# Kernel tuning notes

Hardware: AMD Instinct MI355X
Metric: run time of the kernel (lower is better)

Reference implementation:

```python
import jax, jax.numpy as jnp
import numpy as np

B, C, N, H = 4, 256, 4096, 4
DK = C // H


def _proj(x, w, b):
    # Conv1d with kernel size 1 == per-point linear: [B,C,N] x [O,C] -> [B,O,N]
    return jnp.einsum('oc,bcn->bon', w, x) + b[None, :, None]


def setup_inputs() -> dict:
    key = jax.random.key(0)
    ks = jax.random.split(key, 9)
    s = 1.0 / np.sqrt(C)
    return {
        'x': jax.random.normal(ks[0], (B, C, N), jnp.float32),
        'wq': jax.random.normal(ks[1], (C, C), jnp.float32) * s,
        'bq': jax.random.normal(ks[2], (C,), jnp.float32) * 0.01,
        'wk': jax.random.normal(ks[3], (C, C), jnp.float32) * s,
        'bk': jax.random.normal(ks[4], (C,), jnp.float32) * 0.01,
        'wv': jax.random.normal(ks[5], (C, C), jnp.float32) * s,
        'bv': jax.random.normal(ks[6], (C,), jnp.float32) * 0.01,
        'wp': jax.random.normal(ks[7], (C, C), jnp.float32) * s,
        'bp': jax.random.normal(ks[8], (C,), jnp.float32) * 0.01,
    }


def reference(x, wq, bq, wk, bk, wv, bv, wp, bp):
    b, c, n = x.shape
    q = _proj(x, wq, bq).reshape(b, H, DK, n)
    k = _proj(x, wk, bk).reshape(b, H, DK, n)
    v = _proj(x, wv, bv).reshape(b, H, DK, n)
    scale = 1.0 / jnp.sqrt(jnp.asarray(DK, x.dtype))
    # scores over point pairs: [B,H,N,N]
    scores = jnp.einsum('bhdn,bhdm->bhnm', q, k) * scale
    attn = jax.nn.softmax(scores, axis=-1)
    out = jnp.einsum('bhnm,bhdm->bhdn', attn, v)  # [B,H,DK,N]
    out = out.reshape(b, c, n)
    out = _proj(out, wp, bp)
    return out + x
```

## Files before the change

kernel.cpp:

```cpp
#include <hip/hip_runtime.h>


#define BDIM 4
#define CDIM 256
#define NDIM 4096
#define HDIM 4
#define DKDIM 64
#define NQ   (BDIM * HDIM * NDIM)
#define NSPLIT 2
#define KPERZ (NDIM / NSPLIT)
#define QSCALE 0.18033688011112042f
#define WSZ (CDIM * CDIM)

typedef __bf16 bf16x8 __attribute__((ext_vector_type(8)));
typedef float f32x4 __attribute__((ext_vector_type(4)));
typedef short s16x4 __attribute__((ext_vector_type(4)));
typedef unsigned short u16;
typedef unsigned int u32;

__device__ __forceinline__ u16 f2bf(float f) {
  union { __bf16 h; u16 s; } u; u.h = (__bf16)f; return u.s;
}
__device__ __forceinline__ float bf2f(u16 v) {
  union { u32 u; float f; } x; x.u = (u32)v << 16; return x.f;
}
__device__ __forceinline__ u32 pk2(float a, float b) {
  return (u32)f2bf(a) | ((u32)f2bf(b) << 16);
}
__device__ __forceinline__ void gload16(const u16* g, u16* l) {
  __builtin_amdgcn_global_load_lds(
      (const __attribute__((address_space(1))) void*)g,
      (__attribute__((address_space(3))) void*)l, 16, 0, 0);
}

__global__ __launch_bounds__(256) void wconv_kernel(
    const float* __restrict__ wq, const float* __restrict__ wk,
    const float* __restrict__ wv, const float* __restrict__ wp,
    u16* __restrict__ wb)
{
  const int a = blockIdx.y;
  const float* src = (a == 0) ? wq : (a == 1) ? wk : (a == 2) ? wv : wp;
  const float sc = (a == 0) ? QSCALE : 1.0f;
  const int i = (blockIdx.x * 256 + threadIdx.x) * 8;
  const float4 v0 = *(const float4*)(src + i);
  const float4 v1 = *(const float4*)(src + i + 4);
  union { u32 p[4]; uint4 q; } o;
  o.p[0] = pk2(v0.x * sc, v0.y * sc);
  o.p[1] = pk2(v0.z * sc, v0.w * sc);
  o.p[2] = pk2(v1.x * sc, v1.y * sc);
  o.p[3] = pk2(v1.z * sc, v1.w * sc);
  *(uint4*)(wb + (size_t)a * WSZ + i) = o.q;
}

__global__ __launch_bounds__(256) void xt_kernel(
    const float* __restrict__ x, u16* __restrict__ xT)
{
  const int b = blockIdx.z, c0 = blockIdx.y * 64, n0 = blockIdx.x * 64;
  __shared__ __align__(16) float T[64][68];
  const int t = threadIdx.x;
  {
    const int cr = t >> 4, nc = (t & 15) * 4;
    #pragma unroll
    for (int ci = 0; ci < 4; ++ci) {
      const float4 v = *(const float4*)&x[((size_t)(b * CDIM + c0 + cr + ci * 16)) * NDIM + n0 + nc];
      *(float4*)&T[cr + ci * 16][nc] = v;
    }
  }
  __syncthreads();
  {
    const int n = t >> 2, g = t & 3;
    union { u16 u[16]; uint4 v[2]; } pk;
    #pragma unroll
    for (int u_ = 0; u_ < 16; ++u_) pk.u[u_] = f2bf(T[g * 16 + u_][n]);
    uint4* dst = (uint4*)&xT[((size_t)(b * NDIM + n0 + n)) * CDIM + c0 + g * 16];
    dst[0] = pk.v[0]; dst[1] = pk.v[1];
  }
}

__global__ __launch_bounds__(256, 4) void qkv_kernel(
    const u16* __restrict__ xT, const u16* __restrict__ wb,
    const float* __restrict__ bq, const float* __restrict__ bk,
    const float* __restrict__ bv,
    u16* __restrict__ qT, u16* __restrict__ kT, u16* __restrict__ vB)
{
  const int b = blockIdx.z;
  const int p = blockIdx.y >> 1;
  const int o0 = (blockIdx.y & 1) * 128;
  const int n0 = blockIdx.x * 64;
  const float* bsel = (p == 0) ? bq : (p == 1) ? bk : bv;
  const float wscale = (p == 0) ? QSCALE : 1.0f;

  __shared__ __align__(16) u16 XTs[64][40];
  const int t = threadIdx.x, lane = t & 63, w = t >> 6;
  const int qd = lane >> 4, lm = lane & 15;
  const int sr = t >> 2, sg = (t & 3) * 8;

  const u16* xsrc = xT + ((size_t)(b * NDIM + n0 + sr)) * CDIM + sg;
  const u16* wrow0 = wb + (size_t)p * WSZ + (size_t)(o0 + 32 * w + lm) * CDIM + qd * 8;
  const u16* wrow1 = wrow0 + (size_t)16 * CDIM;

  f32x4 acc[4][2];
  #pragma unroll
  for (int nt = 0; nt < 4; ++nt)
    #pragma unroll
    for (int j = 0; j < 2; ++j) acc[nt][j] = (f32x4){0.f, 0.f, 0.f, 0.f};

  for (int cs = 0; cs < 8; ++cs) {
    const bf16x8 wf0 = *(const bf16x8*)(wrow0 + cs * 32);
    const bf16x8 wf1 = *(const bf16x8*)(wrow1 + cs * 32);
    __syncthreads();
    *(uint4*)&XTs[sr][sg] = *(const uint4*)(xsrc + cs * 32);
    __syncthreads();
    bf16x8 xf[4];
    #pragma unroll
    for (int nt = 0; nt < 4; ++nt) xf[nt] = *(const bf16x8*)&XTs[16 * nt + lm][qd * 8];
    #pragma unroll
    for (int nt = 0; nt < 4; ++nt) {
      if (p < 2) {
        acc[nt][0] = __builtin_amdgcn_mfma_f32_16x16x32_bf16(xf[nt], wf0, acc[nt][0], 0, 0, 0);
        acc[nt][1] = __builtin_amdgcn_mfma_f32_16x16x32_bf16(xf[nt], wf1, acc[nt][1], 0, 0, 0);
      } else {
        acc[nt][0] = __builtin_amdgcn_mfma_f32_16x16x32_bf16(wf0, xf[nt], acc[nt][0], 0, 0, 0);
        acc[nt][1] = __builtin_amdgcn_mfma_f32_16x16x32_bf16(wf1, xf[nt], acc[nt][1], 0, 0, 0);
      }
    }
  }

  if (p < 2) {
    u16* out = (p == 0) ? qT : kT;
    #pragma unroll
    for (int j = 0; j < 2; ++j) {
      const int og = o0 + 32 * w + 16 * j + lm;
      const float bv2 = bsel[og] * wscale;
      #pragma unroll
      for (int nt = 0; nt < 4; ++nt)
        #pragma unroll
        for (int r = 0; r < 4; ++r) {
          const int n = n0 + 16 * nt + 4 * qd + r;
          out[((size_t)(b * NDIM + n)) * CDIM + og] = f2bf(acc[nt][j][r] + bv2);
        }
    }
  } else {
    #pragma unroll
    for (int j = 0; j < 2; ++j) {
      const float4 b4 = *(const float4*)&bsel[o0 + 32 * w + 16 * j + 4 * qd];
      const float bvr[4] = {b4.x, b4.y, b4.z, b4.w};
      #pragma unroll
      for (int nt = 0; nt < 4; ++nt)
        #pragma unroll
        for (int r = 0; r < 4; ++r) {
          const int og = o0 + 32 * w + 16 * j + 4 * qd + r;
          const int n = n0 + 16 * nt + lm;
          vB[((size_t)(b * CDIM + og)) * NDIM + n] = f2bf(acc[nt][j][r] + bvr[r]);
        }
    }
  }
}

__global__ __launch_bounds__(256, 4) void attn_kernel(
    const u16* __restrict__ qT, const u16* __restrict__ kT,
    const u16* __restrict__ vB, u16* __restrict__ Opart,
    float* __restrict__ Lp)
{
  const int bh = blockIdx.y, b = bh >> 2, h = bh & 3;
  const int n0 = blockIdx.x * 128;
  const int z  = blockIdx.z;

  __shared__ __align__(16) u16 KVlds[2][2][64][64];

  const int t = threadIdx.x, lane = t & 63, w = t >> 6;
  const int qd = lane >> 4, lm = lane & 15, l7 = lm & 7;

  bf16x8 qf[2][2];
  {
    const u16* qbase = qT + ((size_t)(b * NDIM) + n0) * CDIM + h * 64;
    #pragma unroll
    for (int s = 0; s < 2; ++s)
      #pragma unroll
      for (int hh = 0; hh < 2; ++hh)
        qf[s][hh] = *(const bf16x8*)(qbase +
            (size_t)(16 * (2 * w + s) + lm) * CDIM + 32 * hh + qd * 8);
  }

  const s16x4 ones = (s16x4){(short)0x3F80, (short)0x3F80, (short)0x3F80, (short)0x3F80};
  f32x4 la[2];
  la[0] = (f32x4){0.f, 0.f, 0.f, 0.f};
  la[1] = (f32x4){0.f, 0.f, 0.f, 0.f};

  f32x4 oa[2][4];
  #pragma unroll
  for (int s = 0; s < 2; ++s)
    #pragma unroll
    for (int dt = 0; dt < 4; ++dt) oa[s][dt] = (f32x4){0.f, 0.f, 0.f, 0.f};

  const int srow = lane >> 3;
  const int swz  = 8 * ((lane & 7) ^ srow);
  const u16* kp0 = kT + ((size_t)(b * NDIM + z * KPERZ + 8 * w + srow)) * CDIM + h * 64 + swz;
  const u16* kp1 = kp0 + (size_t)32 * CDIM;
  const u16* vp0 = vB + ((size_t)(b * CDIM + h * 64 + 8 * w + srow)) * NDIM + z * KPERZ + swz;
  const u16* vp1 = vp0 + (size_t)32 * NDIM;

  {
    u16* kb = &KVlds[0][0][0][0];
    u16* vb2 = &KVlds[0][1][0][0];
    gload16(kp0, kb + w * 512);
    gload16(kp1, kb + (4 + w) * 512);
    gload16(vp0, vb2 + w * 512);
    gload16(vp1, vb2 + (4 + w) * 512);
  }

  #pragma unroll 1
  for (int it = 0; it < KPERZ / 64; ++it) {
    __syncthreads();
    if (it + 1 < KPERZ / 64) {
      const size_t ko = (size_t)(it + 1) * 64 * CDIM;
      const int    vo = (it + 1) * 64;
      u16* kb = &KVlds[(it + 1) & 1][0][0][0];
      u16* vb2 = &KVlds[(it + 1) & 1][1][0][0];
      gload16(kp0 + ko, kb + w * 512);
      gload16(kp1 + ko, kb + (4 + w) * 512);
      gload16(vp0 + vo, vb2 + w * 512);
      gload16(vp1 + vo, vb2 + (4 + w) * 512);
    }
    const u16 (*Kt)[64] = KVlds[it & 1][0];
    const u16 (*Vt)[64] = KVlds[it & 1][1];

    union { u16 u[4]; u32 d[2]; s16x4 v; } pk[2][4];

    #pragma unroll
    for (int nt = 0; nt < 4; ++nt) {
      const bf16x8 kf0 = *(const bf16x8*)&Kt[16 * nt + lm][8 * (qd ^ l7)];
      const bf16x8 kf1 = *(const bf16x8*)&Kt[16 * nt + lm][8 * ((4 + qd) ^ l7)];
      #pragma unroll
      for (int s = 0; s < 2; ++s) {
        f32x4 zz = (f32x4){0.f, 0.f, 0.f, 0.f};
        zz = __builtin_amdgcn_mfma_f32_16x16x32_bf16(kf0, qf[s][0], zz, 0, 0, 0);
        zz = __builtin_amdgcn_mfma_f32_16x16x32_bf16(kf1, qf[s][1], zz, 0, 0, 0);
        const float p0 = __builtin_amdgcn_exp2f(zz[0]);
        const float p1 = __builtin_amdgcn_exp2f(zz[1]);
        const float p2 = __builtin_amdgcn_exp2f(zz[2]);
        const float p3 = __builtin_amdgcn_exp2f(zz[3]);
        pk[s][nt].d[0] = pk2(p0, p1);
        pk[s][nt].d[1] = pk2(p2, p3);
      }
    }

    #pragma unroll
    for (int c = 0; c < 4; ++c) {
      s16x4 av[4];
      #pragma unroll
      for (int dt = 0; dt < 4; ++dt)
        av[dt] = *(const s16x4*)&Vt[16 * dt + lm][(16 * c + 4 * qd) ^ (8 * l7)];
      la[0] = __builtin_amdgcn_mfma_f32_16x16x16bf16_1k(ones, pk[0][c].v, la[0], 0, 0, 0);
      la[1] = __builtin_amdgcn_mfma_f32_16x16x16bf16_1k(ones, pk[1][c].v, la[1], 0, 0, 0);
      #pragma unroll
      for (int dt = 0; dt < 4; ++dt) {
        oa[0][dt] = __builtin_amdgcn_mfma_f32_16x16x16bf16_1k(av[dt], pk[0][c].v, oa[0][dt], 0, 0, 0);
        oa[1][dt] = __builtin_amdgcn_mfma_f32_16x16x16bf16_1k(av[dt], pk[1][c].v, oa[1][dt], 0, 0, 0);
      }
    }
  }

  const float l_i[2] = {la[0][0], la[1][0]};

  __syncthreads();
  u16 (*Ot)[72] = (u16(*)[72])&KVlds[0][0][0][0];
  #pragma unroll
  for (int s = 0; s < 2; ++s) {
    const float inv = 1.0f / l_i[s];
    #pragma unroll
    for (int dt = 0; dt < 4; ++dt)
      #pragma unroll
      for (int r = 0; r < 4; ++r)
        Ot[16 * (2 * w + s) + lm][16 * dt + 4 * qd + r] = f2bf(oa[s][dt][r] * inv);
  }
  if (qd == 0) {
    const size_t lbase = ((size_t)z * (BDIM * HDIM) + bh) * NDIM;
    #pragma unroll
    for (int s = 0; s < 2; ++s)
      Lp[lbase + n0 + 16 * (2 * w + s) + lm] = l_i[s];
  }
  __syncthreads();
  {
    const int r = t >> 1, g = (t & 1) * 32;
    u16* dst = Opart + (((size_t)z * (BDIM * HDIM) + bh) * NDIM + n0 + r) * DKDIM + g;
    const uint4* srcp = (const uint4*)&Ot[r][g];
    uint4* d4 = (uint4*)dst;
    d4[0] = srcp[0]; d4[1] = srcp[1]; d4[2] = srcp[2]; d4[3] = srcp[3];
  }
}

__global__ __launch_bounds__(256, 4) void projout_kernel(
    const u16* __restrict__ Opart, const float* __restrict__ Lp,
    const u16* __restrict__ wb, const float* __restrict__ bp,
    const float* __restrict__ res, float* __restrict__ out)
{
  const int b = blockIdx.z, o0 = blockIdx.y * 128, n0 = blockIdx.x * 64;
  __shared__ __align__(16) u16 XTs[64][40];
  const int t = threadIdx.x, lane = t & 63, w = t >> 6;
  const int qd = lane >> 4, lm = lane & 15;
  const int sr = t >> 2, sg = (t & 3) * 8;

  float wh[4][NSPLIT];
  #pragma unroll
  for (int hh = 0; hh < 4; ++hh) {
    const size_t i0 = ((size_t)(b * HDIM + hh)) * NDIM + n0 + sr;
    float l[NSPLIT], tot = 0.f;
    #pragma unroll
    for (int zz = 0; zz < NSPLIT; ++zz) { l[zz] = Lp[(size_t)zz * NQ + i0]; tot += l[zz]; }
    const float iv = 1.0f / tot;
    #pragma unroll
    for (int zz = 0; zz < NSPLIT; ++zz) wh[hh][zz] = l[zz] * iv;
  }

  const u16* wrow0 = wb + (size_t)3 * WSZ + (size_t)(o0 + 32 * w + lm) * CDIM + qd * 8;
  const u16* wrow1 = wrow0 + (size_t)16 * CDIM;

  f32x4 acc[4][2];
  #pragma unroll
  for (int nt = 0; nt < 4; ++nt)
    #pragma unroll
    for (int j = 0; j < 2; ++j) acc[nt][j] = (f32x4){0.f, 0.f, 0.f, 0.f};

  for (int cs = 0; cs < 8; ++cs) {
    const int c0 = cs * 32;
    const int hh = c0 >> 6;
    const int dk = (c0 & 63) + sg;
    const bf16x8 wf0 = *(const bf16x8*)(wrow0 + c0);
    const bf16x8 wf1 = *(const bf16x8*)(wrow1 + c0);
    __syncthreads();
    {
      const size_t obase = (((size_t)(b * HDIM + hh)) * NDIM + n0 + sr) * DKDIM + dk;
      float v[8] = {0.f, 0.f, 0.f, 0.f, 0.f, 0.f, 0.f, 0.f};
      #pragma unroll
      for (int zz = 0; zz < NSPLIT; ++zz) {
        union { u16 u[8]; uint4 q; } a;
        a.q = *(const uint4*)(Opart + (size_t)zz * NQ * DKDIM + obase);
        const float wz = wh[hh][zz];
        #pragma unroll
        for (int j = 0; j < 8; ++j) v[j] = fmaf(wz, bf2f(a.u[j]), v[j]);
      }
      union { u16 u[8]; uint4 q; } ov;
      #pragma unroll
      for (int j = 0; j < 8; ++j) ov.u[j] = f2bf(v[j]);
      *(uint4*)&XTs[sr][sg] = ov.q;
    }
    __syncthreads();
    bf16x8 xf[4];
    #pragma unroll
    for (int nt = 0; nt < 4; ++nt) xf[nt] = *(const bf16x8*)&XTs[16 * nt + lm][qd * 8];
    #pragma unroll
    for (int nt = 0; nt < 4; ++nt) {
      acc[nt][0] = __builtin_amdgcn_mfma_f32_16x16x32_bf16(wf0, xf[nt], acc[nt][0], 0, 0, 0);
      acc[nt][1] = __builtin_amdgcn_mfma_f32_16x16x32_bf16(wf1, xf[nt], acc[nt][1], 0, 0, 0);
    }
  }

  #pragma unroll
  for (int j = 0; j < 2; ++j) {
    const float4 b4 = *(const float4*)&bp[o0 + 32 * w + 16 * j + 4 * qd];
    const float bvr[4] = {b4.x, b4.y, b4.z, b4.w};
    #pragma unroll
    for (int nt = 0; nt < 4; ++nt)
      #pragma unroll
      for (int r = 0; r < 4; ++r) {
        const int og = o0 + 32 * w + 16 * j + 4 * qd + r;
        const int n = n0 + 16 * nt + lm;
        const size_t idx = ((size_t)(b * CDIM + og)) * NDIM + n;
        out[idx] = acc[nt][j][r] + bvr[r] + res[idx];
      }
  }
}

extern "C" void kernel_launch(void* const* d_in, const int* in_sizes, int n_in,
                              void* d_out, int out_size, void* d_ws, size_t ws_size,
                              hipStream_t stream)
{
  const float* x  = (const float*)d_in[0];
  const float* wq = (const float*)d_in[1];
  const float* bq = (const float*)d_in[2];
  const float* wk = (const float*)d_in[3];
  const float* bk = (const float*)d_in[4];
  const float* wv = (const float*)d_in[5];
  const float* bv = (const float*)d_in[6];
  const float* wp = (const float*)d_in[7];
  const float* bp = (const float*)d_in[8];
  float* out = (float*)d_out;

  const size_t sz = (size_t)BDIM * CDIM * NDIM;
  u16* xTb = (u16*)d_ws;
  u16* qTb = xTb + sz;
  u16* kTb = qTb + sz;
  u16* vBb = kTb + sz;
  u16* Opart = vBb + sz;
  float* Lp = (float*)(Opart + (size_t)NSPLIT * sz);
  u16* wbf = (u16*)(Lp + (size_t)NSPLIT * NQ);

  const dim3 blk(256);
  wconv_kernel<<<dim3(WSZ / (256 * 8), 4, 1), blk, 0, stream>>>(wq, wk, wv, wp, wbf);
  xt_kernel<<<dim3(NDIM / 64, CDIM / 64, BDIM), blk, 0, stream>>>(x, xTb);
  qkv_kernel<<<dim3(NDIM / 64, 6, BDIM), blk, 0, stream>>>(
      xTb, wbf, bq, bk, bv, qTb, kTb, vBb);
  attn_kernel<<<dim3(NDIM / 128, BDIM * HDIM, NSPLIT), blk, 0, stream>>>(
      qTb, kTb, vBb, Opart, Lp);
  projout_kernel<<<dim3(NDIM / 64, 2, BDIM), blk, 0, stream>>>(
      Opart, Lp, wbf, bp, x, out);
}
```

Measured before the change: 200.9 us.

## Use two waves per attention block, each handling 64 query rows

Shrinks the attention block from four waves to two and has each wave process four 16-row query subtiles instead of two. Each K/V fragment read from LDS is then reused across twice as many query rows, which halves the LDS fragment traffic per MFMA and also halves the number of waves that sync per tile. The cost is a larger accumulator set per wave (more registers, lower occupancy, bounded by launch_bounds(128,2)) and each wave issuing twice as many global-to-LDS loads per tile.

```diff
diff --git a/kernel.cpp b/kernel.cpp
--- a/kernel.cpp
+++ b/kernel.cpp
@@ -157,7 +157,7 @@
   }
 }
 
-__global__ __launch_bounds__(256, 4) void attn_kernel(
+__global__ __launch_bounds__(128, 2) void attn_kernel(
     const u16* __restrict__ qT, const u16* __restrict__ kT,
     const u16* __restrict__ vB, u16* __restrict__ Opart,
     float* __restrict__ Lp)
@@ -171,42 +171,41 @@
   const int t = threadIdx.x, lane = t & 63, w = t >> 6;
   const int qd = lane >> 4, lm = lane & 15, l7 = lm & 7;
 
-  bf16x8 qf[2][2];
+  bf16x8 qf[4][2];
   {
     const u16* qbase = qT + ((size_t)(b * NDIM) + n0) * CDIM + h * 64;
     #pragma unroll
-    for (int s = 0; s < 2; ++s)
+    for (int s = 0; s < 4; ++s)
       #pragma unroll
       for (int hh = 0; hh < 2; ++hh)
         qf[s][hh] = *(const bf16x8*)(qbase +
-            (size_t)(16 * (2 * w + s) + lm) * CDIM + 32 * hh + qd * 8);
+            (size_t)(64 * w + 16 * s + lm) * CDIM + 32 * hh + qd * 8);
   }
 
   const s16x4 ones = (s16x4){(short)0x3F80, (short)0x3F80, (short)0x3F80, (short)0x3F80};
-  f32x4 la[2];
-  la[0] = (f32x4){0.f, 0.f, 0.f, 0.f};
-  la[1] = (f32x4){0.f, 0.f, 0.f, 0.f};
-
-  f32x4 oa[2][4];
-  #pragma unroll
-  for (int s = 0; s < 2; ++s)
+  f32x4 la[4];
+  #pragma unroll
+  for (int s = 0; s < 4; ++s) la[s] = (f32x4){0.f, 0.f, 0.f, 0.f};
+
+  f32x4 oa[4][4];
+  #pragma unroll
+  for (int s = 0; s < 4; ++s)
     #pragma unroll
     for (int dt = 0; dt < 4; ++dt) oa[s][dt] = (f32x4){0.f, 0.f, 0.f, 0.f};
 
   const int srow = lane >> 3;
   const int swz  = 8 * ((lane & 7) ^ srow);
   const u16* kp0 = kT + ((size_t)(b * NDIM + z * KPERZ + 8 * w + srow)) * CDIM + h * 64 + swz;
-  const u16* kp1 = kp0 + (size_t)32 * CDIM;
   const u16* vp0 = vB + ((size_t)(b * CDIM + h * 64 + 8 * w + srow)) * NDIM + z * KPERZ + swz;
-  const u16* vp1 = vp0 + (size_t)32 * NDIM;
 
   {
-    u16* kb = &KVlds[0][0][0][0];
-    u16* vb2 = &KVlds[0][1][0][0];
-    gload16(kp0, kb + w * 512);
-    gload16(kp1, kb + (4 + w) * 512);
-    gload16(vp0, vb2 + w * 512);
-    gload16(vp1, vb2 + (4 + w) * 512);
+    u16* kb  = &KVlds[0][0][0][0] + w * 512;
+    u16* vb2 = &KVlds[0][1][0][0] + w * 512;
+    #pragma unroll
+    for (int i = 0; i < 4; ++i) {
+      gload16(kp0 + (size_t)(16 * i) * CDIM, kb + i * 1024);
+      gload16(vp0 + (size_t)(16 * i) * NDIM, vb2 + i * 1024);
+    }
   }
 
   #pragma unroll 1
@@ -215,24 +214,25 @@
     if (it + 1 < KPERZ / 64) {
       const size_t ko = (size_t)(it + 1) * 64 * CDIM;
       const int    vo = (it + 1) * 64;
-      u16* kb = &KVlds[(it + 1) & 1][0][0][0];
-      u16* vb2 = &KVlds[(it + 1) & 1][1][0][0];
-      gload16(kp0 + ko, kb + w * 512);
-      gload16(kp1 + ko, kb + (4 + w) * 512);
-      gload16(vp0 + vo, vb2 + w * 512);
-      gload16(vp1 + vo, vb2 + (4 + w) * 512);
+      u16* kb  = &KVlds[(it + 1) & 1][0][0][0] + w * 512;
+      u16* vb2 = &KVlds[(it + 1) & 1][1][0][0] + w * 512;
+      #pragma unroll
+      for (int i = 0; i < 4; ++i) {
+        gload16(kp0 + ko + (size_t)(16 * i) * CDIM, kb + i * 1024);
+        gload16(vp0 + vo + (size_t)(16 * i) * NDIM, vb2 + i * 1024);
+      }
     }
     const u16 (*Kt)[64] = KVlds[it & 1][0];
     const u16 (*Vt)[64] = KVlds[it & 1][1];
 
-    union { u16 u[4]; u32 d[2]; s16x4 v; } pk[2][4];
+    union { u16 u[4]; u32 d[2]; s16x4 v; } pk[4][4];
 
     #pragma unroll
     for (int nt = 0; nt < 4; ++nt) {
       const bf16x8 kf0 = *(const bf16x8*)&Kt[16 * nt + lm][8 * (qd ^ l7)];
       const bf16x8 kf1 = *(const bf16x8*)&Kt[16 * nt + lm][8 * ((4 + qd) ^ l7)];
       #pragma unroll
-      for (int s = 0; s < 2; ++s) {
+      for (int s = 0; s < 4; ++s) {
         f32x4 zz = (f32x4){0.f, 0.f, 0.f, 0.f};
         zz = __builtin_amdgcn_mfma_f32_16x16x32_bf16(kf0, qf[s][0], zz, 0, 0, 0);
         zz = __builtin_amdgcn_mfma_f32_16x16x32_bf16(kf1, qf[s][1], zz, 0, 0, 0);
@@ -251,42 +251,47 @@
       #pragma unroll
       for (int dt = 0; dt < 4; ++dt)
         av[dt] = *(const s16x4*)&Vt[16 * dt + lm][(16 * c + 4 * qd) ^ (8 * l7)];
-      la[0] = __builtin_amdgcn_mfma_f32_16x16x16bf16_1k(ones, pk[0][c].v, la[0], 0, 0, 0);
-      la[1] = __builtin_amdgcn_mfma_f32_16x16x16bf16_1k(ones, pk[1][c].v, la[1], 0, 0, 0);
-      #pragma unroll
-      for (int dt = 0; dt < 4; ++dt) {
-        oa[0][dt] = __builtin_amdgcn_mfma_f32_16x16x16bf16_1k(av[dt], pk[0][c].v, oa[0][dt], 0, 0, 0);
-        oa[1][dt] = __builtin_amdgcn_mfma_f32_16x16x16bf16_1k(av[dt], pk[1][c].v, oa[1][dt], 0, 0, 0);
-      }
-    }
-  }
-
-  const float l_i[2] = {la[0][0], la[1][0]};
+      #pragma unroll
+      for (int s = 0; s < 4; ++s)
+        la[s] = __builtin_amdgcn_mfma_f32_16x16x16bf16_1k(ones, pk[s][c].v, la[s], 0, 0, 0);
+      #pragma unroll
+      for (int dt = 0; dt < 4; ++dt)
+        #pragma unroll
+        for (int s = 0; s < 4; ++s)
+          oa[s][dt] = __builtin_amdgcn_mfma_f32_16x16x16bf16_1k(av[dt], pk[s][c].v, oa[s][dt], 0, 0, 0);
+    }
+  }
+
+  const float l_i4[4] = {la[0][0], la[1][0], la[2][0], la[3][0]};
 
   __syncthreads();
   u16 (*Ot)[72] = (u16(*)[72])&KVlds[0][0][0][0];
   #pragma unroll
-  for (int s = 0; s < 2; ++s) {
-    const float inv = 1.0f / l_i[s];
+  for (int s = 0; s < 4; ++s) {
+    const float inv = 1.0f / l_i4[s];
     #pragma unroll
     for (int dt = 0; dt < 4; ++dt)
       #pragma unroll
       for (int r = 0; r < 4; ++r)
-        Ot[16 * (2 * w + s) + lm][16 * dt + 4 * qd + r] = f2bf(oa[s][dt][r] * inv);
+        Ot[16 * (4 * w + s) + lm][16 * dt + 4 * qd + r] = f2bf(oa[s][dt][r] * inv);
   }
   if (qd == 0) {
     const size_t lbase = ((size_t)z * (BDIM * HDIM) + bh) * NDIM;
     #pragma unroll
-    for (int s = 0; s < 2; ++s)
-      Lp[lbase + n0 + 16 * (2 * w + s) + lm] = l_i[s];
+    for (int s = 0; s < 4; ++s)
+      Lp[lbase + n0 + 16 * (4 * w + s) + lm] = l_i4[s];
   }
   __syncthreads();
   {
-    const int r = t >> 1, g = (t & 1) * 32;
-    u16* dst = Opart + (((size_t)z * (BDIM * HDIM) + bh) * NDIM + n0 + r) * DKDIM + g;
-    const uint4* srcp = (const uint4*)&Ot[r][g];
-    uint4* d4 = (uint4*)dst;
-    d4[0] = srcp[0]; d4[1] = srcp[1]; d4[2] = srcp[2]; d4[3] = srcp[3];
+    const int g = (t & 1) * 32;
+    #pragma unroll
+    for (int ii = 0; ii < 2; ++ii) {
+      const int r = (t >> 1) + 64 * ii;
+      u16* dst = Opart + (((size_t)z * (BDIM * HDIM) + bh) * NDIM + n0 + r) * DKDIM + g;
+      const uint4* srcp = (const uint4*)&Ot[r][g];
+      uint4* d4 = (uint4*)dst;
+      d4[0] = srcp[0]; d4[1] = srcp[1]; d4[2] = srcp[2]; d4[3] = srcp[3];
+    }
   }
 }
 
@@ -401,7 +406,7 @@
   xt_kernel<<<dim3(NDIM / 64, CDIM / 64, BDIM), blk, 0, stream>>>(x, xTb);
   qkv_kernel<<<dim3(NDIM / 64, 6, BDIM), blk, 0, stream>>>(
       xTb, wbf, bq, bk, bv, qTb, kTb, vBb);
-  attn_kernel<<<dim3(NDIM / 128, BDIM * HDIM, NSPLIT), blk, 0, stream>>>(
+  attn_kernel<<<dim3(NDIM / 128, BDIM * HDIM, NSPLIT), dim3(128), 0, stream>>>(
       qTb, kTb, vBb, Opart, Lp);
   projout_kernel<<<dim3(NDIM / 64, 2, BDIM), blk, 0, stream>>>(
       Opart, Lp, wbf, bp, x, out);
```

Result: no change. 204.3 us (+1.7%).
